# Kernel optimization log

Measured on AMD Instinct MI355X. Metric: run time of the kernel, lower is better.

## Reference

```python
import jax, jax.numpy as jnp
import numpy as np

N_NODES = 100000
N_EDGES = 600000
NODE_DIM = 64
EDGE_DIM = 32
HID = 128
OUT = 24


def setup_inputs() -> dict:
    key = jax.random.key(0)
    ks = jax.random.split(key, 20)

    def w(k, shape):
        return jax.random.normal(k, shape, jnp.float32) * (1.0 / np.sqrt(shape[0]).astype(np.float32))

    inp = {}
    inp["x"] = jax.random.normal(ks[0], (N_NODES, NODE_DIM), jnp.float32)
    inp["edge_index"] = jax.random.randint(ks[1], (2, N_EDGES), 0, N_NODES)
    inp["edge_attr"] = jax.random.normal(ks[2], (N_EDGES, EDGE_DIM), jnp.float32)
    inp["lin1_w"] = w(ks[3], (NODE_DIM, HID)); inp["lin1_b"] = jnp.zeros((HID,), jnp.float32)
    i = 4
    for c in (1, 2, 3):
        inp[f"conv{c}_edge_w"] = w(ks[i], (EDGE_DIM, HID)); inp[f"conv{c}_edge_b"] = jnp.zeros((HID,), jnp.float32)
        inp[f"conv{c}_w1"] = w(ks[i + 1], (HID, HID)); inp[f"conv{c}_b1"] = jnp.zeros((HID,), jnp.float32)
        inp[f"conv{c}_w2"] = w(ks[i + 2], (HID, HID)); inp[f"conv{c}_b2"] = jnp.zeros((HID,), jnp.float32)
        i += 3
    inp["cls_w1"] = w(ks[i], (2 * HID + EDGE_DIM, HID)); inp["cls_b1"] = jnp.zeros((HID,), jnp.float32)
    inp["cls_w2"] = w(ks[i + 1], (HID, OUT)); inp["cls_b2"] = jnp.zeros((OUT,), jnp.float32)
    return inp


def _gine(h, src, dst, e_emb, w1, b1, w2, b2, eps=0.0):
    # GINEConv: out = MLP((1+eps)*x + sum_{j->i} relu(x_j + edge_emb))
    m = jax.nn.relu(h[src] + e_emb)                       # [E, HID] gather + fuse
    agg = jax.ops.segment_sum(m, dst, num_segments=N_NODES)  # scatter-add to dst
    z = (1.0 + eps) * h + agg
    return jax.nn.relu(z @ w1 + b1) @ w2 + b2


def reference(x, edge_index, edge_attr,
              lin1_w, lin1_b,
              conv1_edge_w, conv1_edge_b, conv1_w1, conv1_b1, conv1_w2, conv1_b2,
              conv2_edge_w, conv2_edge_b, conv2_w1, conv2_b1, conv2_w2, conv2_b2,
              conv3_edge_w, conv3_edge_b, conv3_w1, conv3_b1, conv3_w2, conv3_b2,
              cls_w1, cls_b1, cls_w2, cls_b2):
    src, dst = edge_index[0], edge_index[1]
    h = x @ lin1_w + lin1_b                               # [N, HID]
    layers = [
        (conv1_edge_w, conv1_edge_b, conv1_w1, conv1_b1, conv1_w2, conv1_b2),
        (conv2_edge_w, conv2_edge_b, conv2_w1, conv2_b1, conv2_w2, conv2_b2),
        (conv3_edge_w, conv3_edge_b, conv3_w1, conv3_b1, conv3_w2, conv3_b2),
    ]
    for ew, eb, w1, b1, w2, b2 in layers:
        e_emb = edge_attr @ ew + eb                       # [E, HID]
        h = jax.nn.relu(_gine(h, src, dst, e_emb, w1, b1, w2, b2))
    edge_feat = jnp.concatenate([h[src], h[dst], edge_attr], axis=-1)  # [E, 2*HID+EDGE_DIM]
    return jax.nn.relu(edge_feat @ cls_w1 + cls_b1) @ cls_w2 + cls_b2  # [E, OUT]
```

## Files before the change

kernel.cpp:

```cpp
#include <hip/hip_runtime.h>

#define N_NODES 100000
#define N_EDGES 600000
#define NODE_DIM 64
#define EDGE_DIM 32
#define HID 128
#define OUT_DIM 24

typedef short short8 __attribute__((ext_vector_type(8)));
typedef short short4v __attribute__((ext_vector_type(4)));
typedef float f32x4 __attribute__((ext_vector_type(4)));

#define MFMA16(a, b, c) __builtin_amdgcn_mfma_f32_16x16x32_bf16(a, b, c, 0, 0, 0)

__device__ inline unsigned short f2bf(float f) {
  unsigned u = __float_as_uint(f);
  u += 0x7FFFu + ((u >> 16) & 1u);
  return (unsigned short)(u >> 16);
}
__device__ inline float bf2f(unsigned short b) {
  return __uint_as_float(((unsigned)b) << 16);
}

#define OFF_CW1T 0
#define OFF_CW2T 36864
#define OFF_LAYER(c) (40960 + (c)*65536)
#define OFF_EWT(c) (237568 + (c)*8192)
#define W_TOTAL 262144

__global__ __launch_bounds__(256) void prep_weights(
    const float* __restrict__ cw1, const float* __restrict__ cw2,
    const float* __restrict__ l0w1, const float* __restrict__ l0w2,
    const float* __restrict__ l1w1, const float* __restrict__ l1w2,
    const float* __restrict__ l2w1, const float* __restrict__ l2w2,
    const float* __restrict__ e0w, const float* __restrict__ e1w,
    const float* __restrict__ e2w,
    unsigned short* __restrict__ wb) {
  int i = blockIdx.x * 256 + threadIdx.x;
  if (i < 36864) {
    int n = i / 288, k = i % 288;
    wb[OFF_CW1T + i] = f2bf(cw1[k * 128 + n]);
  }
  int j = i - 36864;
  if (j >= 0 && j < 4096) {
    int n = j / 128, k = j % 128;
    wb[OFF_CW2T + j] = f2bf(n < 24 ? cw2[k * 24 + n] : 0.f);
  }
  int t = i - 40960;
  if (t >= 0 && t < 3 * 32768) {
    int c = t / 32768, u = t % 32768;
    const float* w = (u < 16384) ? (c == 0 ? l0w1 : c == 1 ? l1w1 : l2w1)
                                 : (c == 0 ? l0w2 : c == 1 ? l1w2 : l2w2);
    int v = u & 16383;
    int n = v >> 7, k = v & 127;
    float val = w[k * 128 + n];
    unsigned short hi = f2bf(val);
    unsigned short lo = f2bf(val - bf2f(hi));
    int base = OFF_LAYER(c) + (u < 16384 ? 0 : 32768);
    wb[base + v] = hi;
    wb[base + 16384 + v] = lo;
  }
  int p = i - 139264;
  if (p >= 0 && p < 3 * 8192) {
    int c = p / 8192, u = p % 8192;
    int v = u & 4095;
    int s = v >> 3, jj = v & 7;
    int ntile = s >> 6, kgrp = (s >> 4) & 3, nrow = s & 15;
    int n = ntile * 16 + nrow, k = kgrp * 8 + jj;
    const float* ew = (c == 0 ? e0w : c == 1 ? e1w : e2w);
    float val = ew[k * 128 + n];
    unsigned short hi = f2bf(val);
    wb[OFF_EWT(c) + u] = (u < 4096) ? hi : f2bf(val - bf2f(hi));
  }
}

__global__ __launch_bounds__(256) void lin1_kernel(
    const float* __restrict__ x, const float* __restrict__ w,
    const float* __restrict__ b, float* __restrict__ h,
    unsigned short* __restrict__ hbf) {
  __shared__ float4 smem4[3072];
  float* sA = (float*)smem4;
  float* sB = (float*)smem4 + 4096;
  int tid = threadIdx.x;
  int tn = tid & 31, tm = tid >> 5;
  int mbase = blockIdx.x * 64;

  for (int i = tid; i < 1024; i += 256) {
    int m = i & 63, k4 = (i >> 6) << 2;
    int row = mbase + m; if (row >= N_NODES) row = N_NODES - 1;
    float4 v = *(const float4*)(x + (size_t)row * NODE_DIM + k4);
    sA[(k4 + 0) * 64 + m] = v.x; sA[(k4 + 1) * 64 + m] = v.y;
    sA[(k4 + 2) * 64 + m] = v.z; sA[(k4 + 3) * 64 + m] = v.w;
  }
  for (int i = tid; i < 2048; i += 256)
    *(float4*)&sB[i * 4] = ((const float4*)w)[i];
  __syncthreads();

  float acc[8][4] = {};
#pragma unroll 8
  for (int k = 0; k < 64; ++k) {
    float4 a0 = *(float4*)&sA[k * 64 + tm * 8];
    float4 a1 = *(float4*)&sA[k * 64 + tm * 8 + 4];
    float4 bv = *(float4*)&sB[k * 128 + tn * 4];
    float av[8] = {a0.x, a0.y, a0.z, a0.w, a1.x, a1.y, a1.z, a1.w};
    float bb[4] = {bv.x, bv.y, bv.z, bv.w};
#pragma unroll
    for (int i = 0; i < 8; ++i)
#pragma unroll
      for (int jj = 0; jj < 4; ++jj) acc[i][jj] = fmaf(av[i], bb[jj], acc[i][jj]);
  }
  float4 bv = *(const float4*)(b + tn * 4);
#pragma unroll
  for (int i = 0; i < 8; ++i) {
    int row = mbase + tm * 8 + i;
    if (row < N_NODES) {
      float4 o = {acc[i][0] + bv.x, acc[i][1] + bv.y, acc[i][2] + bv.z, acc[i][3] + bv.w};
      *(float4*)(h + (size_t)row * HID + tn * 4) = o;
      short4v pk = {(short)f2bf(o.x), (short)f2bf(o.y), (short)f2bf(o.z), (short)f2bf(o.w)};
      *(short4v*)(hbf + (size_t)row * HID + tn * 4) = pk;
    }
  }
}

__global__ __launch_bounds__(256) void hist_kernel(
    const int* __restrict__ dst, int* __restrict__ counts) {
  int e = blockIdx.x * 256 + threadIdx.x;
  if (e < N_EDGES) atomicAdd(&counts[dst[e]], 1);
}

#define SCAN_BLK 98
__global__ __launch_bounds__(256) void scan_partial(
    const int* __restrict__ cnt, int* __restrict__ partial) {
  __shared__ int sdata[256];
  int b = blockIdx.x, t = threadIdx.x;
  int sum = 0;
  for (int i = t; i < 1024; i += 256) {
    int idx = b * 1024 + i;
    sum += (idx < N_NODES) ? cnt[idx] : 0;
  }
  sdata[t] = sum; __syncthreads();
  for (int s = 128; s > 0; s >>= 1) {
    if (t < s) sdata[t] += sdata[t + s];
    __syncthreads();
  }
  if (t == 0) partial[b] = sdata[0];
}

__global__ void scan_sums(const int* __restrict__ partial,
                          int* __restrict__ partialScan, int* __restrict__ rowptr) {
  if (threadIdx.x == 0) {
    int acc = 0;
    for (int i = 0; i < SCAN_BLK; ++i) { partialScan[i] = acc; acc += partial[i]; }
    rowptr[N_NODES] = acc;
  }
}

__global__ __launch_bounds__(256) void scan_final(
    const int* __restrict__ cnt, const int* __restrict__ partialScan,
    int* __restrict__ rowptr, int* __restrict__ cur) {
  __shared__ int sdata[256];
  int b = blockIdx.x, t = threadIdx.x;
  int i0 = b * 1024 + t * 4;
  int c[4]; int s = 0;
#pragma unroll
  for (int j = 0; j < 4; ++j) {
    c[j] = (i0 + j < N_NODES) ? cnt[i0 + j] : 0;
    s += c[j];
  }
  sdata[t] = s; __syncthreads();
  for (int d = 1; d < 256; d <<= 1) {
    int u = (t >= d) ? sdata[t - d] : 0;
    __syncthreads();
    sdata[t] += u;
    __syncthreads();
  }
  int off = sdata[t] - s + partialScan[b];
#pragma unroll
  for (int j = 0; j < 4; ++j) {
    int idx = i0 + j;
    if (idx < N_NODES) { rowptr[idx] = off; cur[idx] = off; off += c[j]; }
  }
}

__global__ __launch_bounds__(256) void scatter_kernel(
    const int* __restrict__ dst, const int* __restrict__ src,
    int* __restrict__ cur, int* __restrict__ perm,
    int* __restrict__ srcp, int* __restrict__ dstp) {
  int e = blockIdx.x * 256 + threadIdx.x;
  if (e < N_EDGES) {
    int d = dst[e];
    int slot = atomicAdd(&cur[d], 1);
    perm[slot] = e;
    srcp[slot] = src[e];
    dstp[slot] = d;
  }
}

__global__ __launch_bounds__(256) void build_eafrag(
    const float* __restrict__ ea, const int* __restrict__ perm,
    unsigned short* __restrict__ frag) {
  int slot = blockIdx.x * 256 + threadIdx.x;
  if (slot >= N_EDGES) return;
  int e = perm[slot];
  const float4* row = (const float4*)(ea + (size_t)e * EDGE_DIM);
  unsigned short* dp = frag + ((size_t)(slot >> 7)) * 4096 +
                       (size_t)(((slot & 127) >> 4)) * 512 + (slot & 15) * 8;
#pragma unroll
  for (int kg = 0; kg < 4; ++kg) {
    float4 v0 = row[kg * 2], v1 = row[kg * 2 + 1];
    short8 pk = {(short)f2bf(v0.x), (short)f2bf(v0.y), (short)f2bf(v0.z), (short)f2bf(v0.w),
                 (short)f2bf(v1.x), (short)f2bf(v1.y), (short)f2bf(v1.z), (short)f2bf(v1.w)};
    *(short8*)(dp + kg * 128) = pk;
  }
}

__global__ __launch_bounds__(256) void edge_agg_kernel(
    const unsigned short* __restrict__ hbf, const unsigned short* __restrict__ eafrag,
    const int* __restrict__ srcp, const int* __restrict__ dstp,
    const unsigned short* __restrict__ ewt, const float* __restrict__ eb,
    float* __restrict__ agg) {
  __shared__ float emb[128 * 132];
  __shared__ int sidx[128];
  __shared__ int sdst[128];
  int tid = threadIdx.x, lane = tid & 63, wave = tid >> 6;
  int wm = wave & 1, wn = wave >> 1;
  int sbase = blockIdx.x * 128;
  int nrows = N_EDGES - sbase; if (nrows > 128) nrows = 128;
  if (tid < 128) {
    int sl = sbase + tid;
    sidx[tid] = (sl < N_EDGES) ? srcp[sl] : 0;
    sdst[tid] = (sl < N_EDGES) ? dstp[sl] : -1;
  }
  const short8* Af = (const short8*)(eafrag) + (size_t)blockIdx.x * 512;
  const short8* Bh = (const short8*)(ewt);
  const short8* Bl = (const short8*)(ewt + 4096);
  short8 af[4], bh[4], bl[4];
#pragma unroll
  for (int mt = 0; mt < 4; ++mt) af[mt] = Af[(wm * 4 + mt) * 64 + lane];
#pragma unroll
  for (int nt = 0; nt < 4; ++nt) {
    bh[nt] = Bh[(wn * 4 + nt) * 64 + lane];
    bl[nt] = Bl[(wn * 4 + nt) * 64 + lane];
  }
  const f32x4 zf = {0.f, 0.f, 0.f, 0.f};
  f32x4 acc[4][4];
#pragma unroll
  for (int mt = 0; mt < 4; ++mt)
#pragma unroll
    for (int nt = 0; nt < 4; ++nt) {
      acc[mt][nt] = MFMA16(af[mt], bh[nt], zf);
      acc[mt][nt] = MFMA16(af[mt], bl[nt], acc[mt][nt]);
    }
  int q = lane >> 4, r = lane & 15;
#pragma unroll
  for (int nt = 0; nt < 4; ++nt) {
    int n = wn * 64 + nt * 16 + r;
    float ebv = eb[n];
#pragma unroll
    for (int mt = 0; mt < 4; ++mt) {
      int rowb = (wm * 4 + mt) * 16 + q * 4;
#pragma unroll
      for (int i2 = 0; i2 < 4; ++i2)
        emb[(rowb + i2) * 132 + n] = acc[mt][nt][i2] + ebv;
    }
  }
  __syncthreads();
  {
    int r0 = wave * 32;
#pragma unroll 4
    for (int rr = 0; rr < 32; ++rr) {
      int row = r0 + rr;
      int s = sidx[row];
      unsigned u = *(const unsigned*)(hbf + (size_t)s * HID + lane * 2);
      float2 ev = *(float2*)(emb + row * 132 + lane * 2);
      ev.x = fmaxf(ev.x + bf2f((unsigned short)u), 0.f);
      ev.y = fmaxf(ev.y + bf2f((unsigned short)(u >> 16)), 0.f);
      *(float2*)(emb + row * 132 + lane * 2) = ev;
    }
  }
  __syncthreads();
  {
    int hh = tid >> 7;
    int col = tid & 127;
    int rbeg = hh * 64;
    int rend = rbeg + 64; if (rend > nrows) rend = nrows;
    if (rbeg < rend) {
      float a = 0.f;
      int cnode = sdst[rbeg];
      bool atomic_first = true;
      for (int rr = rbeg; rr < rend; ++rr) {
        int node = sdst[rr];
        if (node != cnode) {
          if (atomic_first) atomicAdd(&agg[(size_t)cnode * HID + col], a);
          else agg[(size_t)cnode * HID + col] = a;
          a = 0.f; cnode = node; atomic_first = false;
        }
        a += emb[rr * 132 + col];
      }
      atomicAdd(&agg[(size_t)cnode * HID + col], a);
    }
  }
}

__global__ __launch_bounds__(256) void agg_gather_kernel(
    const float* __restrict__ h, const float* __restrict__ ea,
    const int* __restrict__ srcp, const int* __restrict__ perm,
    const int* __restrict__ rowptr,
    const float* __restrict__ ew, const float* __restrict__ eb,
    float* __restrict__ agg) {
  int tid = threadIdx.x, lane = tid & 63;
  int wid = blockIdx.x * 4 + (tid >> 6);
  int nwaves = gridDim.x * 4;
  const float2* ew2 = (const float2*)ew;
  float2 ebv = *(const float2*)(eb + lane * 2);

  for (int node = wid; node < N_NODES; node += nwaves) {
    int beg = rowptr[node], end = rowptr[node + 1];
    float2 acc = {0.f, 0.f};
    for (int i = beg; i < end; ++i) {
      int s0 = srcp[i];
      int e0 = perm[i];
      float2 h0 = *(const float2*)(h + (size_t)s0 * HID + lane * 2);
      const float4* ea0 = (const float4*)(ea + (size_t)e0 * EDGE_DIM);
      float2 m0 = ebv;
#pragma unroll
      for (int k4 = 0; k4 < 8; ++k4) {
        float4 a0 = ea0[k4];
        float a0v[4] = {a0.x, a0.y, a0.z, a0.w};
#pragma unroll
        for (int j = 0; j < 4; ++j) {
          float2 w = ew2[(k4 * 4 + j) * 64 + lane];
          m0.x = fmaf(a0v[j], w.x, m0.x);
          m0.y = fmaf(a0v[j], w.y, m0.y);
        }
      }
      acc.x += fmaxf(m0.x + h0.x, 0.f);
      acc.y += fmaxf(m0.y + h0.y, 0.f);
    }
    *(float2*)(agg + (size_t)node * HID + lane * 2) = acc;
  }
}

__global__ __launch_bounds__(256) void mlp_mfma(
    const float* __restrict__ h, const float* __restrict__ agg,
    const unsigned short* __restrict__ wl,
    const float* __restrict__ b1, const float* __restrict__ b2,
    float* __restrict__ hout, unsigned short* __restrict__ hbfout) {
  __shared__ unsigned short lds[40960];
  unsigned short* sAh = lds;
  unsigned short* sAl = lds + 4096;
  unsigned short* sBh = lds + 8192;
  unsigned short* sBl = lds + 12288;
  unsigned short* t1h = lds;
  unsigned short* t1l = lds + 16384;
  unsigned short* sB2h = lds + 32768;
  unsigned short* sB2l = lds + 36864;
  const unsigned short* w1h = wl;
  const unsigned short* w1l = wl + 16384;
  const unsigned short* w2h = wl + 32768;
  const unsigned short* w2l = wl + 49152;
  int tid = threadIdx.x, lane = tid & 63, wave = tid >> 6;
  int wm = wave & 1, wn = wave >> 1;
  int mbase = blockIdx.x * 128;
  const f32x4 zf = {0.f, 0.f, 0.f, 0.f};

  f32x4 acc[4][4];
#pragma unroll
  for (int a = 0; a < 4; ++a)
#pragma unroll
    for (int bq = 0; bq < 4; ++bq) acc[a][bq] = zf;

  for (int c = 0; c < 4; ++c) {
    __syncthreads();
#pragma unroll
    for (int it = 0; it < 4; ++it) {
      int idx = it * 256 + tid;
      int m = idx >> 3, k4 = (idx & 7) * 4;
      int row = mbase + m; if (row >= N_NODES) row = N_NODES - 1;
      size_t g = (size_t)row * HID + c * 32 + k4;
      float4 hv = *(const float4*)(h + g);
      float4 av = *(const float4*)(agg + g);
      float z0 = hv.x + av.x, z1 = hv.y + av.y, z2 = hv.z + av.z, z3 = hv.w + av.w;
      unsigned short h0 = f2bf(z0), h1 = f2bf(z1), h2 = f2bf(z2), h3 = f2bf(z3);
      int slot = ((m >> 4) * 4 + (k4 >> 3)) * 16 + (m & 15);
      int off = slot * 8 + (k4 & 7);
      short4v ph = {(short)h0, (short)h1, (short)h2, (short)h3};
      short4v pl = {(short)f2bf(z0 - bf2f(h0)), (short)f2bf(z1 - bf2f(h1)),
                    (short)f2bf(z2 - bf2f(h2)), (short)f2bf(z3 - bf2f(h3))};
      *(short4v*)(sAh + off) = ph;
      *(short4v*)(sAl + off) = pl;
    }
#pragma unroll
    for (int it = 0; it < 2; ++it) {
      int s = it * 256 + tid;
      int ntile = s >> 6, kgrp = (s >> 4) & 3, nrow = s & 15;
      int goff = (ntile * 16 + nrow) * 128 + c * 32 + kgrp * 8;
      *(short8*)(sBh + s * 8) = *(const short8*)(w1h + goff);
      *(short8*)(sBl + s * 8) = *(const short8*)(w1l + goff);
    }
    __syncthreads();
    short8 ah[4], al[4], bh[4], bl[4];
#pragma unroll
    for (int mt = 0; mt < 4; ++mt) {
      ah[mt] = *(short8*)(sAh + ((wm * 4 + mt) * 64 + lane) * 8);
      al[mt] = *(short8*)(sAl + ((wm * 4 + mt) * 64 + lane) * 8);
    }
#pragma unroll
    for (int nt = 0; nt < 4; ++nt) {
      bh[nt] = *(short8*)(sBh + ((wn * 4 + nt) * 64 + lane) * 8);
      bl[nt] = *(short8*)(sBl + ((wn * 4 + nt) * 64 + lane) * 8);
    }
#pragma unroll
    for (int mt = 0; mt < 4; ++mt)
#pragma unroll
      for (int nt = 0; nt < 4; ++nt) {
        acc[mt][nt] = MFMA16(ah[mt], bh[nt], acc[mt][nt]);
        acc[mt][nt] = MFMA16(ah[mt], bl[nt], acc[mt][nt]);
        acc[mt][nt] = MFMA16(al[mt], bh[nt], acc[mt][nt]);
      }
  }
  __syncthreads();
  int q = lane >> 4, r = lane & 15;
#pragma unroll
  for (int nt = 0; nt < 4; ++nt) {
    int n = wn * 64 + nt * 16 + r;
    float b1v = b1[n];
    int kgrp = n >> 3, jj = n & 7;
#pragma unroll
    for (int mt = 0; mt < 4; ++mt) {
      int mtg = wm * 4 + mt;
#pragma unroll
      for (int i2 = 0; i2 < 4; ++i2) {
        int mrow = q * 4 + i2;
        float val = fmaxf(acc[mt][nt][i2] + b1v, 0.f);
        unsigned short hi = f2bf(val);
        int idx = ((mtg * 16 + kgrp) * 16 + mrow) * 8 + jj;
        t1h[idx] = hi;
        t1l[idx] = f2bf(val - bf2f(hi));
      }
    }
  }

  f32x4 acc2[4][4];
#pragma unroll
  for (int a = 0; a < 4; ++a)
#pragma unroll
    for (int bq = 0; bq < 4; ++bq) acc2[a][bq] = zf;

  for (int kc = 0; kc < 4; ++kc) {
    __syncthreads();
#pragma unroll
    for (int it = 0; it < 2; ++it) {
      int s = it * 256 + tid;
      int ntile = s >> 6, kgrp = (s >> 4) & 3, nrow = s & 15;
      int goff = (ntile * 16 + nrow) * 128 + kc * 32 + kgrp * 8;
      *(short8*)(sB2h + s * 8) = *(const short8*)(w2h + goff);
      *(short8*)(sB2l + s * 8) = *(const short8*)(w2l + goff);
    }
    __syncthreads();
    short8 ah[4], al[4], bh[4], bl[4];
#pragma unroll
    for (int mt = 0; mt < 4; ++mt) {
      int mtg = wm * 4 + mt;
      int idx = ((mtg * 16 + kc * 4 + q) * 16 + r) * 8;
      ah[mt] = *(short8*)(t1h + idx);
      al[mt] = *(short8*)(t1l + idx);
    }
#pragma unroll
    for (int nt = 0; nt < 4; ++nt) {
      bh[nt] = *(short8*)(sB2h + ((wn * 4 + nt) * 64 + lane) * 8);
      bl[nt] = *(short8*)(sB2l + ((wn * 4 + nt) * 64 + lane) * 8);
    }
#pragma unroll
    for (int mt = 0; mt < 4; ++mt)
#pragma unroll
      for (int nt = 0; nt < 4; ++nt) {
        acc2[mt][nt] = MFMA16(ah[mt], bh[nt], acc2[mt][nt]);
        acc2[mt][nt] = MFMA16(ah[mt], bl[nt], acc2[mt][nt]);
        acc2[mt][nt] = MFMA16(al[mt], bh[nt], acc2[mt][nt]);
      }
  }
#pragma unroll
  for (int nt = 0; nt < 4; ++nt) {
    int n = wn * 64 + nt * 16 + r;
    float b2v = b2[n];
#pragma unroll
    for (int mt = 0; mt < 4; ++mt) {
      int mtg = wm * 4 + mt;
#pragma unroll
      for (int i2 = 0; i2 < 4; ++i2) {
        int row = mbase + mtg * 16 + q * 4 + i2;
        if (row < N_NODES) {
          float val = fmaxf(acc2[mt][nt][i2] + b2v, 0.f);
          hout[(size_t)row * HID + n] = val;
          hbfout[(size_t)row * HID + n] = f2bf(val);
        }
      }
    }
  }
}

__global__ __launch_bounds__(256) void cls_mfma(
    const unsigned short* __restrict__ hbf, const float* __restrict__ ea,
    const int* __restrict__ src, const int* __restrict__ dst,
    const unsigned short* __restrict__ w1t, const unsigned short* __restrict__ w2t,
    const float* __restrict__ b1, const float* __restrict__ b2,
    float* __restrict__ out) {
  __shared__ unsigned short lds[20480];
  unsigned short* sA = lds;
  unsigned short* sB = lds + 4096;
  unsigned short* t1 = lds;
  unsigned short* sB2 = lds + 16384;
  __shared__ int sidx[256];
  int tid = threadIdx.x, lane = tid & 63, wave = tid >> 6;
  int wm = wave & 1, wn = wave >> 1;
  int ebase = blockIdx.x * 128;
  const f32x4 zf = {0.f, 0.f, 0.f, 0.f};

  {
    int e0 = ebase + (tid & 127);
    if (e0 >= N_EDGES) e0 = N_EDGES - 1;
    sidx[tid] = (tid < 128 ? src : dst)[e0];
  }

  f32x4 acc[4][4];
#pragma unroll
  for (int a = 0; a < 4; ++a)
#pragma unroll
    for (int bq = 0; bq < 4; ++bq) acc[a][bq] = zf;

  for (int c = 0; c < 9; ++c) {
    __syncthreads();
    if (c < 8) {
#pragma unroll
      for (int it = 0; it < 2; ++it) {
        int idx = it * 256 + tid;
        int kgrp = idx >> 7, m = idx & 127;
        int node = (c < 4) ? sidx[m] : sidx[128 + m];
        int cc = (c & 3) * 32;
        short8 v = *(const short8*)(hbf + (size_t)node * HID + cc + kgrp * 8);
        *(short8*)(sA + (((m >> 4) * 4 + kgrp) * 16 + (m & 15)) * 8) = v;
      }
    } else {
#pragma unroll
      for (int it = 0; it < 4; ++it) {
        int idx = it * 256 + tid;
        int m = idx >> 3, k4 = (idx & 7) * 4;
        int e8 = ebase + m; if (e8 >= N_EDGES) e8 = N_EDGES - 1;
        float4 v = *(const float4*)(ea + (size_t)e8 * EDGE_DIM + k4);
        int slot = ((m >> 4) * 4 + (k4 >> 3)) * 16 + (m & 15);
        short4v pk = {(short)f2bf(v.x), (short)f2bf(v.y), (short)f2bf(v.z), (short)f2bf(v.w)};
        *(short4v*)(sA + slot * 8 + (k4 & 7)) = pk;
      }
    }
#pragma unroll
    for (int it = 0; it < 2; ++it) {
      int s = it * 256 + tid;
      int ntile = s >> 6, kgrp = (s >> 4) & 3, nrow = s & 15;
      *(short8*)(sB + s * 8) = *(const short8*)(w1t + (ntile * 16 + nrow) * 288 + c * 32 + kgrp * 8);
    }
    __syncthreads();
    short8 af[4], bfv[4];
#pragma unroll
    for (int mt = 0; mt < 4; ++mt)
      af[mt] = *(short8*)(sA + ((wm * 4 + mt) * 64 + lane) * 8);
#pragma unroll
    for (int nt = 0; nt < 4; ++nt)
      bfv[nt] = *(short8*)(sB + ((wn * 4 + nt) * 64 + lane) * 8);
#pragma unroll
    for (int mt = 0; mt < 4; ++mt)
#pragma unroll
      for (int nt = 0; nt < 4; ++nt)
        acc[mt][nt] = MFMA16(af[mt], bfv[nt], acc[mt][nt]);
  }
  __syncthreads();
  int q = lane >> 4, r = lane & 15;
#pragma unroll
  for (int nt = 0; nt < 4; ++nt) {
    int n = wn * 64 + nt * 16 + r;
    float b1v = b1[n];
    int kgrp = n >> 3, jj = n & 7;
#pragma unroll
    for (int mt = 0; mt < 4; ++mt) {
      int mtg = wm * 4 + mt;
#pragma unroll
      for (int i2 = 0; i2 < 4; ++i2) {
        int mrow = q * 4 + i2;
        float val = fmaxf(acc[mt][nt][i2] + b1v, 0.f);
        t1[((mtg * 16 + kgrp) * 16 + mrow) * 8 + jj] = f2bf(val);
      }
    }
  }
#pragma unroll
  for (int it = 0; it < 2; ++it) {
    int s = it * 256 + tid;
    int ntile = s >> 8, kgrp = (s >> 4) & 15, nrow = s & 15;
    *(short8*)(sB2 + s * 8) = *(const short8*)(w2t + (ntile * 16 + nrow) * 128 + kgrp * 8);
  }
  __syncthreads();

  f32x4 acc2[2][2];
  acc2[0][0] = zf; acc2[0][1] = zf; acc2[1][0] = zf; acc2[1][1] = zf;
#pragma unroll
  for (int kc = 0; kc < 4; ++kc) {
    short8 a0 = *(short8*)(t1 + (((wave * 2 + 0) * 16 + kc * 4 + q) * 16 + r) * 8);
    short8 a1 = *(short8*)(t1 + (((wave * 2 + 1) * 16 + kc * 4 + q) * 16 + r) * 8);
    short8 b0 = *(short8*)(sB2 + ((0 * 16 + kc * 4 + q) * 16 + r) * 8);
    short8 b1f = *(short8*)(sB2 + ((1 * 16 + kc * 4 + q) * 16 + r) * 8);
    acc2[0][0] = MFMA16(a0, b0, acc2[0][0]);
    acc2[0][1] = MFMA16(a0, b1f, acc2[0][1]);
    acc2[1][0] = MFMA16(a1, b0, acc2[1][0]);
    acc2[1][1] = MFMA16(a1, b1f, acc2[1][1]);
  }
#pragma unroll
  for (int nt2 = 0; nt2 < 2; ++nt2) {
    int n = nt2 * 16 + r;
    float b2v = (n < OUT_DIM) ? b2[n] : 0.f;
#pragma unroll
    for (int mt2 = 0; mt2 < 2; ++mt2) {
      int mtg = wave * 2 + mt2;
#pragma unroll
      for (int i2 = 0; i2 < 4; ++i2) {
        int e = ebase + mtg * 16 + q * 4 + i2;
        if (n < OUT_DIM && e < N_EDGES)
          out[(size_t)e * OUT_DIM + n] = acc2[mt2][nt2][i2] + b2v;
      }
    }
  }
}

extern "C" void kernel_launch(void* const* d_in, const int* in_sizes, int n_in,
                              void* d_out, int out_size, void* d_ws, size_t ws_size,
                              hipStream_t stream) {
  const float* x = (const float*)d_in[0];
  const int* ei = (const int*)d_in[1];
  const float* ea = (const float*)d_in[2];
  const float* lin1_w = (const float*)d_in[3];
  const float* lin1_b = (const float*)d_in[4];
  const int* src = ei;
  const int* dst = ei + N_EDGES;

  const size_t NH = (size_t)N_NODES * HID;
  float* bufA = (float*)d_ws;
  float* bufB = bufA + NH;
  int* ibase = (int*)(bufB + NH);
  int* rowptr = ibase;
  int* cur = ibase + 100004;
  int* counts = ibase + 200004;
  int* perm = ibase + 300004;
  int* partial = ibase + 900004;
  int* partialScan = ibase + 900132;
  int* srcp = ibase + 900260;
  int* dstp = ibase + 1500260;
  unsigned short* hbf = (unsigned short*)(ibase + 2100264);
  unsigned short* eafrag = hbf + (size_t)N_NODES * HID;
  size_t need = (size_t)((char*)(eafrag + (size_t)N_EDGES * EDGE_DIM) - (char*)d_ws) +
                (size_t)W_TOTAL * 2 + 4096;
  bool big = ws_size >= need;
  unsigned short* wbase = (unsigned short*)((((uintptr_t)d_ws + ws_size) - (size_t)W_TOTAL * 2) & ~(uintptr_t)255);

  prep_weights<<<(163840 + 255) / 256, 256, 0, stream>>>(
      (const float*)d_in[23], (const float*)d_in[25],
      (const float*)d_in[7], (const float*)d_in[9],
      (const float*)d_in[13], (const float*)d_in[15],
      (const float*)d_in[19], (const float*)d_in[21],
      (const float*)d_in[5], (const float*)d_in[11], (const float*)d_in[17],
      wbase);

  lin1_kernel<<<(N_NODES + 63) / 64, 256, 0, stream>>>(x, lin1_w, lin1_b, bufA, hbf);

  hipMemsetAsync(counts, 0, N_NODES * sizeof(int), stream);
  hist_kernel<<<(N_EDGES + 255) / 256, 256, 0, stream>>>(dst, counts);
  scan_partial<<<SCAN_BLK, 256, 0, stream>>>(counts, partial);
  scan_sums<<<1, 64, 0, stream>>>(partial, partialScan, rowptr);
  scan_final<<<SCAN_BLK, 256, 0, stream>>>(counts, partialScan, rowptr, cur);
  scatter_kernel<<<(N_EDGES + 255) / 256, 256, 0, stream>>>(dst, src, cur, perm, srcp, dstp);
  if (big)
    build_eafrag<<<(N_EDGES + 255) / 256, 256, 0, stream>>>(ea, perm, eafrag);

  float* hcur = bufA;
  float* aux = bufB;
  for (int c = 0; c < 3; ++c) {
    const float* ew = (const float*)d_in[5 + c * 6 + 0];
    const float* eb = (const float*)d_in[5 + c * 6 + 1];
    const float* b1 = (const float*)d_in[5 + c * 6 + 3];
    const float* b2 = (const float*)d_in[5 + c * 6 + 5];
    if (big) {
      hipMemsetAsync(aux, 0, NH * sizeof(float), stream);
      edge_agg_kernel<<<(N_EDGES + 127) / 128, 256, 0, stream>>>(
          hbf, eafrag, srcp, dstp, wbase + OFF_EWT(c), eb, aux);
    } else {
      agg_gather_kernel<<<2048, 256, 0, stream>>>(
          hcur, ea, srcp, perm, rowptr, ew, eb, aux);
    }
    mlp_mfma<<<(N_NODES + 127) / 128, 256, 0, stream>>>(
        hcur, aux, wbase + OFF_LAYER(c), b1, b2, aux, hbf);
    float* tmp = hcur; hcur = aux; aux = tmp;
  }

  const float* cb1 = (const float*)d_in[24];
  const float* cb2 = (const float*)d_in[26];
  cls_mfma<<<(N_EDGES + 127) / 128, 256, 0, stream>>>(
      hbf, ea, src, dst, wbase + OFF_CW1T, wbase + OFF_CW2T, cb1, cb2, (float*)d_out);
}
```

Measured before the change: 1.024 ms.

## Widen edge gather loads and process two K-chunks per stage in classifier

The edge message loop now has each lane handle four columns with 8-byte bf16 gathers and float4 LDS accesses, covering two rows per wave iteration. The classifier GEMM is restructured to stage two 32-wide K chunks per barrier pair, loading full 128-byte node row segments with 16-byte gathers into an XOR-swizzled LDS layout. The edge_attr chunk is handled separately at the end. This halves the number of syncthreads in the first GEMM and improves gather coalescing, at the cost of more LDS use and more complex indexing.

```diff
diff --git a/kernel.cpp b/kernel.cpp
--- a/kernel.cpp
+++ b/kernel.cpp
@@ -267,15 +267,18 @@
   __syncthreads();
   {
     int r0 = wave * 32;
-#pragma unroll 4
-    for (int rr = 0; rr < 32; ++rr) {
-      int row = r0 + rr;
+    int cl = (lane & 31) * 4;
+#pragma unroll 8
+    for (int rr = 0; rr < 16; ++rr) {
+      int row = r0 + rr * 2 + (lane >> 5);
       int s = sidx[row];
-      unsigned u = *(const unsigned*)(hbf + (size_t)s * HID + lane * 2);
-      float2 ev = *(float2*)(emb + row * 132 + lane * 2);
-      ev.x = fmaxf(ev.x + bf2f((unsigned short)u), 0.f);
-      ev.y = fmaxf(ev.y + bf2f((unsigned short)(u >> 16)), 0.f);
-      *(float2*)(emb + row * 132 + lane * 2) = ev;
+      uint2 u = *(const uint2*)(hbf + (size_t)s * HID + cl);
+      float4 ev = *(float4*)(emb + row * 132 + cl);
+      ev.x = fmaxf(ev.x + bf2f((unsigned short)u.x), 0.f);
+      ev.y = fmaxf(ev.y + bf2f((unsigned short)(u.x >> 16)), 0.f);
+      ev.z = fmaxf(ev.z + bf2f((unsigned short)u.y), 0.f);
+      ev.w = fmaxf(ev.w + bf2f((unsigned short)(u.y >> 16)), 0.f);
+      *(float4*)(emb + row * 132 + cl) = ev;
     }
   }
   __syncthreads();
@@ -507,13 +510,14 @@
     const float* __restrict__ b1, const float* __restrict__ b2,
     float* __restrict__ out) {
   __shared__ unsigned short lds[20480];
-  unsigned short* sA = lds;
-  unsigned short* sB = lds + 4096;
+  unsigned short* sA2 = lds;
+  unsigned short* sBp = lds + 8192;
   unsigned short* t1 = lds;
   unsigned short* sB2 = lds + 16384;
   __shared__ int sidx[256];
   int tid = threadIdx.x, lane = tid & 63, wave = tid >> 6;
   int wm = wave & 1, wn = wave >> 1;
+  int q = lane >> 4, r = lane & 15;
   int ebase = blockIdx.x * 128;
   const f32x4 zf = {0.f, 0.f, 0.f, 0.f};
 
@@ -529,44 +533,74 @@
 #pragma unroll
     for (int bq = 0; bq < 4; ++bq) acc[a][bq] = zf;
 
-  for (int c = 0; c < 9; ++c) {
-    __syncthreads();
-    if (c < 8) {
-#pragma unroll
-      for (int it = 0; it < 2; ++it) {
-        int idx = it * 256 + tid;
-        int kgrp = idx >> 7, m = idx & 127;
-        int node = (c < 4) ? sidx[m] : sidx[128 + m];
-        int cc = (c & 3) * 32;
-        short8 v = *(const short8*)(hbf + (size_t)node * HID + cc + kgrp * 8);
-        *(short8*)(sA + (((m >> 4) * 4 + kgrp) * 16 + (m & 15)) * 8) = v;
-      }
-    } else {
-#pragma unroll
-      for (int it = 0; it < 4; ++it) {
-        int idx = it * 256 + tid;
-        int m = idx >> 3, k4 = (idx & 7) * 4;
-        int e8 = ebase + m; if (e8 >= N_EDGES) e8 = N_EDGES - 1;
-        float4 v = *(const float4*)(ea + (size_t)e8 * EDGE_DIM + k4);
-        int slot = ((m >> 4) * 4 + (k4 >> 3)) * 16 + (m & 15);
-        short4v pk = {(short)f2bf(v.x), (short)f2bf(v.y), (short)f2bf(v.z), (short)f2bf(v.w)};
-        *(short4v*)(sA + slot * 8 + (k4 & 7)) = pk;
-      }
-    }
-#pragma unroll
-    for (int it = 0; it < 2; ++it) {
-      int s = it * 256 + tid;
+  for (int cp = 0; cp < 4; ++cp) {
+    __syncthreads();
+#pragma unroll
+    for (int it = 0; it < 4; ++it) {
+      int idx = it * 256 + tid;
+      int m = idx >> 3, sub = idx & 7;
+      int node = (cp < 2) ? sidx[m] : sidx[128 + m];
+      int eoff = (cp & 1) * 64;
+      short8 v = *(const short8*)(hbf + (size_t)node * HID + eoff + sub * 8);
+      int ch = sub >> 2, kg = sub & 3;
+      *(short8*)(sA2 + ch * 4096 +
+                 (((m >> 4) * 4 + kg) * 16 + ((m & 15) ^ sub)) * 8) = v;
+    }
+#pragma unroll
+    for (int it = 0; it < 4; ++it) {
+      int s2 = it * 256 + tid;
+      int ch = s2 >> 9, s = s2 & 511;
       int ntile = s >> 6, kgrp = (s >> 4) & 3, nrow = s & 15;
-      *(short8*)(sB + s * 8) = *(const short8*)(w1t + (ntile * 16 + nrow) * 288 + c * 32 + kgrp * 8);
-    }
-    __syncthreads();
+      int c = cp * 2 + ch;
+      *(short8*)(sBp + ch * 4096 + s * 8) =
+          *(const short8*)(w1t + (ntile * 16 + nrow) * 288 + c * 32 + kgrp * 8);
+    }
+    __syncthreads();
+#pragma unroll
+    for (int ch = 0; ch < 2; ++ch) {
+      short8 af[4], bfv[4];
+#pragma unroll
+      for (int mt = 0; mt < 4; ++mt)
+        af[mt] = *(short8*)(sA2 + ch * 4096 +
+                            (((wm * 4 + mt) * 4 + q) * 16 + (r ^ (ch * 4 + q))) * 8);
+#pragma unroll
+      for (int nt = 0; nt < 4; ++nt)
+        bfv[nt] = *(short8*)(sBp + ch * 4096 + ((wn * 4 + nt) * 64 + lane) * 8);
+#pragma unroll
+      for (int mt = 0; mt < 4; ++mt)
+#pragma unroll
+        for (int nt = 0; nt < 4; ++nt)
+          acc[mt][nt] = MFMA16(af[mt], bfv[nt], acc[mt][nt]);
+    }
+  }
+  __syncthreads();
+#pragma unroll
+  for (int it = 0; it < 4; ++it) {
+    int idx = it * 256 + tid;
+    int m = idx >> 3, k4 = (idx & 7) * 4;
+    int e8 = ebase + m; if (e8 >= N_EDGES) e8 = N_EDGES - 1;
+    float4 v = *(const float4*)(ea + (size_t)e8 * EDGE_DIM + k4);
+    int kg = k4 >> 3;
+    int slot = ((m >> 4) * 4 + kg) * 16 + ((m & 15) ^ kg);
+    short4v pk = {(short)f2bf(v.x), (short)f2bf(v.y), (short)f2bf(v.z), (short)f2bf(v.w)};
+    *(short4v*)(sA2 + slot * 8 + (k4 & 7)) = pk;
+  }
+#pragma unroll
+  for (int it = 0; it < 2; ++it) {
+    int s = it * 256 + tid;
+    int ntile = s >> 6, kgrp = (s >> 4) & 3, nrow = s & 15;
+    *(short8*)(sBp + s * 8) =
+        *(const short8*)(w1t + (ntile * 16 + nrow) * 288 + 8 * 32 + kgrp * 8);
+  }
+  __syncthreads();
+  {
     short8 af[4], bfv[4];
 #pragma unroll
     for (int mt = 0; mt < 4; ++mt)
-      af[mt] = *(short8*)(sA + ((wm * 4 + mt) * 64 + lane) * 8);
+      af[mt] = *(short8*)(sA2 + (((wm * 4 + mt) * 4 + q) * 16 + (r ^ q)) * 8);
 #pragma unroll
     for (int nt = 0; nt < 4; ++nt)
-      bfv[nt] = *(short8*)(sB + ((wn * 4 + nt) * 64 + lane) * 8);
+      bfv[nt] = *(short8*)(sBp + ((wn * 4 + nt) * 64 + lane) * 8);
 #pragma unroll
     for (int mt = 0; mt < 4; ++mt)
 #pragma unroll
@@ -574,7 +608,6 @@
         acc[mt][nt] = MFMA16(af[mt], bfv[nt], acc[mt][nt]);
   }
   __syncthreads();
-  int q = lane >> 4, r = lane & 15;
 #pragma unroll
   for (int nt = 0; nt < 4; ++nt) {
     int n = wn * 64 + nt * 16 + r;
```

After: 985.1 us. 3.8% less time.
